# Kernel optimization log

Hardware: AMD Instinct MI355X
Metric: run time of the kernel (lower is better)

Reference implementation:

```python
import jax, jax.numpy as jnp
import numpy as np

B, N, D, H, L = 8, 128, 512, 8, 2
DK = D // H
FF = 4 * D
EPS = 1e-5  # torch LayerNorm default


def _ln(x, g, b):
    m = jnp.mean(x, axis=-1, keepdims=True)
    v = jnp.mean((x - m) ** 2, axis=-1, keepdims=True)
    return (x - m) * jax.lax.rsqrt(v + EPS) * g + b


def setup_inputs() -> dict:
    key = jax.random.key(0)
    ks = iter(jax.random.split(key, 48))
    s = 0.02

    def w(shape):
        return s * jax.random.normal(next(ks), shape, jnp.float32)

    inp = {
        "node_features": jax.random.normal(next(ks), (B, N, D), jnp.float32),
        "edge_features": jax.random.normal(next(ks), (B, N, N, D), jnp.float32),
        "adjacency": (jax.random.uniform(next(ks), (B, N, N)) < 0.3).astype(jnp.float32),
    }
    for name, shape in [("Wq", (L, D, D)), ("Wk", (L, D, D)), ("Wv", (L, D, D)),
                        ("Wo", (L, D, D)), ("Wg", (L, D, D)),
                        ("Wf1", (L, D, FF)), ("Wf2", (L, FF, D))]:
        inp[name] = w(shape)
    for name, shape in [("bq", (L, D)), ("bk", (L, D)), ("bv", (L, D)), ("bo", (L, D)),
                        ("bg", (L, D)), ("bf1", (L, FF)), ("bf2", (L, D))]:
        inp[name] = jnp.zeros(shape, jnp.float32)
    for name in ["ln1", "ln2", "ln3"]:
        inp[name + "_g"] = jnp.ones((L, D), jnp.float32)
        inp[name + "_b"] = jnp.zeros((L, D), jnp.float32)
    return inp


def _forward(node_features, edge_features, adjacency,
             Wq, bq, Wk, bk, Wv, bv, Wo, bo, ln1_g, ln1_b,
             Wg, bg, ln2_g, ln2_b, Wf1, bf1, Wf2, bf2, ln3_g, ln3_b):
    # edge bias is the mean over the feature dim, broadcast over heads: (B,1,N,N)
    edge_bias = jnp.mean(edge_features, axis=-1)[:, None]
    # adjacency-normalized GCN operator: (A + I) / row-degree (clamped to >=1)
    adj = adjacency + jnp.eye(N, dtype=adjacency.dtype)
    adj_norm = adj / jnp.clip(jnp.sum(adj, axis=-1, keepdims=True), 1.0, None)
    scale = 1.0 / np.sqrt(DK).astype(np.float32)

    x = node_features
    for l in range(L):
        # --- multi-head graph attention (dropout = identity in eval) ---
        q = (x @ Wq[l] + bq[l]).reshape(B, N, H, DK).transpose(0, 2, 1, 3)
        k = (x @ Wk[l] + bk[l]).reshape(B, N, H, DK).transpose(0, 2, 1, 3)
        v = (x @ Wv[l] + bv[l]).reshape(B, N, H, DK).transpose(0, 2, 1, 3)
        scores = jnp.einsum('bhnd,bhmd->bhnm', q, k) * scale + edge_bias
        attn = jax.nn.softmax(scores, axis=-1)
        ctx = jnp.einsum('bhnm,bhmd->bhnd', attn, v).transpose(0, 2, 1, 3).reshape(B, N, D)
        x = _ln(x + ctx @ Wo[l] + bo[l], ln1_g[l], ln1_b[l])
        # --- GCN aggregation with residual ---
        agg = jnp.einsum('bnm,bmd->bnd', adj_norm, x)
        x = _ln(x + jax.nn.relu(agg @ Wg[l] + bg[l]), ln2_g[l], ln2_b[l])
        # --- FFN with residual ---
        f = jax.nn.relu(x @ Wf1[l] + bf1[l]) @ Wf2[l] + bf2[l]
        x = _ln(x + f, ln3_g[l], ln3_b[l])
    return x


def reference(node_features, edge_features, adjacency,
              Wq, bq, Wk, bk, Wv, bv, Wo, bo, ln1_g, ln1_b,
              Wg, bg, ln2_g, ln2_b, Wf1, bf1, Wf2, bf2, ln3_g, ln3_b):
    return _forward(node_features, edge_features, adjacency,
                    Wq, bq, Wk, bk, Wv, bv, Wo, bo, ln1_g, ln1_b,
                    Wg, bg, ln2_g, ln2_b, Wf1, bf1, Wf2, bf2, ln3_g, ln3_b)
```

## Files before the change

### kernel.cpp

```cpp
#include <hip/hip_runtime.h>

#define B_  8
#define N_  128
#define D_  512
#define H_  8
#define DK_ 64
#define FF_ 2048
#define L_  2
#define EPS_ 1e-5f

#define BND  (B_*N_*D_)
#define BNN  (B_*N_*N_)
#define BNFF (B_*N_*FF_)
#define DD   (D_*D_)
#define DFF  (D_*FF_)
#define LAYER_SHORTS (10L*DD + 4L*DFF)

typedef __attribute__((ext_vector_type(8))) short short8;
typedef __attribute__((ext_vector_type(4))) float f32x4;

__device__ __forceinline__ unsigned short bf16h(float f) {
    unsigned u = __float_as_uint(f);
    return (unsigned short)((u + 0x7FFFu + ((u >> 16) & 1u)) >> 16);
}
__device__ __forceinline__ float bf16f(unsigned short h) {
    return __uint_as_float((unsigned)h << 16);
}

__global__ __launch_bounds__(256) void edge_mean_kernel(
    const float* __restrict__ ef, float* __restrict__ eb)
{
    int wid  = (blockIdx.x * blockDim.x + threadIdx.x) >> 6;
    int lane = threadIdx.x & 63;
    if (wid >= BNN) return;
    const float* p = ef + (long)wid * D_;
    float4 a = *(const float4*)&p[lane * 4];
    float4 b = *(const float4*)&p[256 + lane * 4];
    float s = a.x + a.y + a.z + a.w + b.x + b.y + b.z + b.w;
    #pragma unroll
    for (int off = 32; off; off >>= 1) s += __shfl_xor(s, off);
    if (lane == 0) eb[wid] = s * (1.0f / (float)D_);
}

__global__ __launch_bounds__(128) void adj_norm_kernel(
    const float* __restrict__ adj, float* __restrict__ an)
{
    int bi = blockIdx.x;
    int j  = threadIdx.x;
    int i  = bi & (N_ - 1);
    const float* row = adj + (long)bi * N_;
    float v = row[j] + (j == i ? 1.0f : 0.0f);
    float s = v;
    #pragma unroll
    for (int off = 32; off; off >>= 1) s += __shfl_xor(s, off);
    __shared__ float partial[2];
    if ((threadIdx.x & 63) == 0) partial[threadIdx.x >> 6] = s;
    __syncthreads();
    float tot = partial[0] + partial[1];
    tot = fmaxf(tot, 1.0f);
    an[(long)bi * N_ + j] = v / tot;
}

__global__ __launch_bounds__(256) void wconv_kernel(
    const float* __restrict__ W, unsigned short* __restrict__ Whi,
    unsigned short* __restrict__ Wlo, int K, int N)
{
    __shared__ ushort2 tile[64][65];
    int t = threadIdx.x;
    int k0 = blockIdx.y << 6, n0 = blockIdx.x << 6;
    #pragma unroll
    for (int p = 0; p < 4; ++p) {
        int k = (t >> 4) + (p << 4);
        int n = (t & 15) << 2;
        float4 v = *(const float4*)&W[(long)(k0 + k) * N + n0 + n];
        float vv[4] = {v.x, v.y, v.z, v.w};
        #pragma unroll
        for (int j = 0; j < 4; ++j) {
            unsigned short h = bf16h(vv[j]);
            unsigned short l = bf16h(vv[j] - bf16f(h));
            tile[k][n + j] = make_ushort2(h, l);
        }
    }
    __syncthreads();
    #pragma unroll
    for (int p = 0; p < 4; ++p) {
        int n = (t >> 4) + (p << 4);
        int k = (t & 15) << 2;
        ushort2 e0 = tile[k][n], e1 = tile[k + 1][n];
        ushort2 e2 = tile[k + 2][n], e3 = tile[k + 3][n];
        *(ushort4*)&Whi[(long)(n0 + n) * K + k0 + k] = make_ushort4(e0.x, e1.x, e2.x, e3.x);
        *(ushort4*)&Wlo[(long)(n0 + n) * K + k0 + k] = make_ushort4(e0.y, e1.y, e2.y, e3.y);
    }
}

__global__ __launch_bounds__(256) void gemm_mfma_kernel(
    const float* __restrict__ A,
    const unsigned short* __restrict__ WTbase, long wstride,
    const float* __restrict__ bias0, const float* __restrict__ bias1,
    const float* __restrict__ bias2,
    float* __restrict__ C, long cstride,
    int M, int N, int K, int relu)
{
    __shared__ __align__(16) unsigned short Ah[64][40];
    __shared__ __align__(16) unsigned short Al[64][40];

    int t = threadIdx.x;
    int z = blockIdx.z;
    const unsigned short* Whi = WTbase + (long)z * wstride;
    const unsigned short* Wlo = Whi + (long)N * K;
    const float* bias = (z == 0) ? bias0 : (z == 1 ? bias1 : bias2);
    float* Cb = C + (long)z * cstride;

    int m0 = blockIdx.y << 6, n0 = blockIdx.x << 6;
    int wv = t >> 6, lane = t & 63;
    int lr = lane & 15, lk = lane >> 4;

    int sr = t >> 2;
    int sk = (t & 3) << 3;
    const float* Ap = &A[(long)(m0 + sr) * K + sk];

    f32x4 acc[4] = {{0.f,0.f,0.f,0.f},{0.f,0.f,0.f,0.f},
                    {0.f,0.f,0.f,0.f},{0.f,0.f,0.f,0.f}};

    for (int k0 = 0; k0 < K; k0 += 32) {
        float4 va = *(const float4*)(Ap + k0);
        float4 vb = *(const float4*)(Ap + k0 + 4);
        float f[8] = {va.x, va.y, va.z, va.w, vb.x, vb.y, vb.z, vb.w};
        unsigned short hh[8], ll[8];
        #pragma unroll
        for (int i = 0; i < 8; ++i) {
            hh[i] = bf16h(f[i]);
            ll[i] = bf16h(f[i] - bf16f(hh[i]));
        }
        __syncthreads();
        *(ushort4*)&Ah[sr][sk]     = make_ushort4(hh[0], hh[1], hh[2], hh[3]);
        *(ushort4*)&Ah[sr][sk + 4] = make_ushort4(hh[4], hh[5], hh[6], hh[7]);
        *(ushort4*)&Al[sr][sk]     = make_ushort4(ll[0], ll[1], ll[2], ll[3]);
        *(ushort4*)&Al[sr][sk + 4] = make_ushort4(ll[4], ll[5], ll[6], ll[7]);
        __syncthreads();

        short8 ah = *(const short8*)&Ah[(wv << 4) + lr][lk << 3];
        short8 al = *(const short8*)&Al[(wv << 4) + lr][lk << 3];
        #pragma unroll
        for (int nf = 0; nf < 4; ++nf) {
            long off = (long)(n0 + (nf << 4) + lr) * K + k0 + (lk << 3);
            short8 bh = *(const short8*)(Whi + off);
            short8 bl = *(const short8*)(Wlo + off);
            acc[nf] = __builtin_amdgcn_mfma_f32_16x16x32_bf16(ah, bh, acc[nf], 0, 0, 0);
            acc[nf] = __builtin_amdgcn_mfma_f32_16x16x32_bf16(ah, bl, acc[nf], 0, 0, 0);
            acc[nf] = __builtin_amdgcn_mfma_f32_16x16x32_bf16(al, bh, acc[nf], 0, 0, 0);
        }
    }

    #pragma unroll
    for (int nf = 0; nf < 4; ++nf) {
        int col = n0 + (nf << 4) + lr;
        float bi = bias ? bias[col] : 0.f;
        #pragma unroll
        for (int r = 0; r < 4; ++r) {
            int row = m0 + (wv << 4) + (lk << 2) + r;
            float o = acc[nf][r] + bi;
            if (relu) o = fmaxf(o, 0.f);
            Cb[(long)row * N + col] = o;
        }
    }
}

__global__ __launch_bounds__(256) void gemm_kernel(
    const float* __restrict__ A, const float* __restrict__ W,
    const float* __restrict__ bias, float* __restrict__ C,
    int M, int N, int K,
    long sA, long sW, long sC, int relu)
{
    __shared__ float As[16][64];
    __shared__ float Bs[16][64];

    int tid = threadIdx.x;
    int bx = blockIdx.x, by = blockIdx.y, bz = blockIdx.z;
    const float* Ab = A + (long)bz * sA;
    const float* Wb = W + (long)bz * sW;
    float*       Cb = C + (long)bz * sC;

    int tx = tid & 15, ty = tid >> 4;
    int arow = tid >> 2, acol = (tid & 3) * 4;
    int brow = tid >> 4, bcol = (tid & 15) * 4;

    float acc[4][4] = {};

    for (int k0 = 0; k0 < K; k0 += 16) {
        float4 av = *(const float4*)&Ab[(long)(by * 64 + arow) * K + k0 + acol];
        float4 bv = *(const float4*)&Wb[(long)(k0 + brow) * N + bx * 64 + bcol];
        __syncthreads();
        As[acol + 0][arow] = av.x;
        As[acol + 1][arow] = av.y;
        As[acol + 2][arow] = av.z;
        As[acol + 3][arow] = av.w;
        *(float4*)&Bs[brow][bcol] = bv;
        __syncthreads();
        #pragma unroll
        for (int kk = 0; kk < 16; ++kk) {
            float a0 = As[kk][ty * 4 + 0];
            float a1 = As[kk][ty * 4 + 1];
            float a2 = As[kk][ty * 4 + 2];
            float a3 = As[kk][ty * 4 + 3];
            float4 b = *(float4*)&Bs[kk][tx * 4];
            acc[0][0] += a0 * b.x; acc[0][1] += a0 * b.y; acc[0][2] += a0 * b.z; acc[0][3] += a0 * b.w;
            acc[1][0] += a1 * b.x; acc[1][1] += a1 * b.y; acc[1][2] += a1 * b.z; acc[1][3] += a1 * b.w;
            acc[2][0] += a2 * b.x; acc[2][1] += a2 * b.y; acc[2][2] += a2 * b.z; acc[2][3] += a2 * b.w;
            acc[3][0] += a3 * b.x; acc[3][1] += a3 * b.y; acc[3][2] += a3 * b.z; acc[3][3] += a3 * b.w;
        }
    }

    int col = bx * 64 + tx * 4;
    float4 bo = {0.f, 0.f, 0.f, 0.f};
    if (bias) bo = *(const float4*)&bias[col];
    #pragma unroll
    for (int i = 0; i < 4; ++i) {
        int row = by * 64 + ty * 4 + i;
        float4 o;
        o.x = acc[i][0] + bo.x;
        o.y = acc[i][1] + bo.y;
        o.z = acc[i][2] + bo.z;
        o.w = acc[i][3] + bo.w;
        if (relu) {
            o.x = fmaxf(o.x, 0.f); o.y = fmaxf(o.y, 0.f);
            o.z = fmaxf(o.z, 0.f); o.w = fmaxf(o.w, 0.f);
        }
        *(float4*)&Cb[(long)row * N + col] = o;
    }
}

#define LDP 129
__global__ __launch_bounds__(256) void attn_kernel(
    const float* __restrict__ q, const float* __restrict__ k,
    const float* __restrict__ v, const float* __restrict__ eb,
    float* __restrict__ ctx)
{
    __shared__ float KT[DK_][LDP];
    __shared__ float Vs[N_][DK_];
    __shared__ float qs[2][DK_];
    __shared__ float ps[2][N_];
    __shared__ float red[2][2];
    __shared__ float cpar[2][2][DK_];

    int bh = blockIdx.x;
    int rg = blockIdx.y;
    int b  = bh >> 3, hh = bh & 7;
    int t  = threadIdx.x;

    {
        int d  = t & 63;
        int jb = t >> 6;
        const float* kb = k + ((long)b * N_) * D_ + hh * DK_;
        const float* vb = v + ((long)b * N_) * D_ + hh * DK_;
        for (int j = jb; j < N_; j += 4) {
            KT[d][j] = kb[(long)j * D_ + d];
            Vs[j][d] = vb[(long)j * D_ + d];
        }
    }
    __syncthreads();

    int sub  = t >> 7;
    int j    = t & 127;
    int lane = t & 63;
    int wh   = (t >> 6) & 1;
    int d    = t & 63;
    const float scale = 0.125f;

    for (int it = 0; it < 16; ++it) {
        int row0 = rg * 32 + it * 2;
        if (t < 128)
            qs[t >> 6][t & 63] =
                q[((long)b * N_ + row0 + (t >> 6)) * D_ + hh * DK_ + (t & 63)];
        __syncthreads();

        int row = row0 + sub;
        float s = 0.f;
        #pragma unroll
        for (int dd = 0; dd < DK_; ++dd) s += qs[sub][dd] * KT[dd][j];
        s = s * scale + eb[((long)b * N_ + row) * N_ + j];

        float m = s;
        #pragma unroll
        for (int off = 32; off; off >>= 1) m = fmaxf(m, __shfl_xor(m, off));
        if (lane == 0) red[sub][wh] = m;
        __syncthreads();
        m = fmaxf(red[sub][0], red[sub][1]);

        float p  = expf(s - m);
        float su = p;
        #pragma unroll
        for (int off = 32; off; off >>= 1) su += __shfl_xor(su, off);
        __syncthreads();
        if (lane == 0) red[sub][wh] = su;
        __syncthreads();
        su = red[sub][0] + red[sub][1];

        ps[sub][j] = p / su;
        __syncthreads();

        float acc = 0.f;
        int j0 = wh * 64;
        #pragma unroll
        for (int jj = 0; jj < 64; ++jj) acc += ps[sub][j0 + jj] * Vs[j0 + jj][d];
        cpar[sub][wh][d] = acc;
        __syncthreads();
        if (wh == 0)
            ctx[((long)b * N_ + row) * D_ + hh * DK_ + d] =
                cpar[sub][0][d] + cpar[sub][1][d];
        __syncthreads();
    }
}

__global__ __launch_bounds__(64) void ln_residual_kernel(
    float* __restrict__ x, const float* __restrict__ y,
    const float* __restrict__ g, const float* __restrict__ bb)
{
    int row  = blockIdx.x;
    int lane = threadIdx.x;
    float* xr = x + (long)row * D_;
    const float* yr = y + (long)row * D_;

    float4 a0 = *(const float4*)&xr[lane * 4];
    float4 a1 = *(const float4*)&xr[256 + lane * 4];
    float4 b0 = *(const float4*)&yr[lane * 4];
    float4 b1 = *(const float4*)&yr[256 + lane * 4];

    float v0[8] = {a0.x + b0.x, a0.y + b0.y, a0.z + b0.z, a0.w + b0.w,
                   a1.x + b1.x, a1.y + b1.y, a1.z + b1.z, a1.w + b1.w};

    float s1 = 0.f, s2 = 0.f;
    #pragma unroll
    for (int i = 0; i < 8; ++i) { s1 += v0[i]; s2 += v0[i] * v0[i]; }
    #pragma unroll
    for (int off = 32; off; off >>= 1) {
        s1 += __shfl_xor(s1, off);
        s2 += __shfl_xor(s2, off);
    }
    float mean = s1 * (1.0f / (float)D_);
    float var  = s2 * (1.0f / (float)D_) - mean * mean;
    float rstd = rsqrtf(var + EPS_);

    float4 g0 = *(const float4*)&g[lane * 4];
    float4 g1 = *(const float4*)&g[256 + lane * 4];
    float4 q0 = *(const float4*)&bb[lane * 4];
    float4 q1 = *(const float4*)&bb[256 + lane * 4];

    float4 o0, o1;
    o0.x = (v0[0] - mean) * rstd * g0.x + q0.x;
    o0.y = (v0[1] - mean) * rstd * g0.y + q0.y;
    o0.z = (v0[2] - mean) * rstd * g0.z + q0.z;
    o0.w = (v0[3] - mean) * rstd * g0.w + q0.w;
    o1.x = (v0[4] - mean) * rstd * g1.x + q1.x;
    o1.y = (v0[5] - mean) * rstd * g1.y + q1.y;
    o1.z = (v0[6] - mean) * rstd * g1.z + q1.z;
    o1.w = (v0[7] - mean) * rstd * g1.w + q1.w;

    *(float4*)&xr[lane * 4]       = o0;
    *(float4*)&xr[256 + lane * 4] = o1;
}

extern "C" void kernel_launch(void* const* d_in, const int* in_sizes, int n_in,
                              void* d_out, int out_size, void* d_ws, size_t ws_size,
                              hipStream_t stream)
{
    const float* node = (const float*)d_in[0];
    const float* edge = (const float*)d_in[1];
    const float* adj  = (const float*)d_in[2];
    const float* Wq = (const float*)d_in[3];
    const float* Wk = (const float*)d_in[4];
    const float* Wv = (const float*)d_in[5];
    const float* Wo = (const float*)d_in[6];
    const float* Wg = (const float*)d_in[7];
    const float* Wf1 = (const float*)d_in[8];
    const float* Wf2 = (const float*)d_in[9];
    const float* bq = (const float*)d_in[10];
    const float* bk = (const float*)d_in[11];
    const float* bv = (const float*)d_in[12];
    const float* bo = (const float*)d_in[13];
    const float* bg = (const float*)d_in[14];
    const float* bf1 = (const float*)d_in[15];
    const float* bf2 = (const float*)d_in[16];
    const float* ln1g = (const float*)d_in[17];
    const float* ln1b = (const float*)d_in[18];
    const float* ln2g = (const float*)d_in[19];
    const float* ln2b = (const float*)d_in[20];
    const float* ln3g = (const float*)d_in[21];
    const float* ln3b = (const float*)d_in[22];

    float* x  = (float*)d_out;
    float* ws = (float*)d_ws;
    float* eb   = ws;
    float* an   = eb + BNN;
    float* q    = an + BNN;
    float* kk   = q + BND;
    float* vv   = kk + BND;
    float* ctx  = vv + BND;
    float* hbuf = q;
    float* tbuf = ctx + BND;
    unsigned short* wcv = (unsigned short*)(tbuf + BND);

    hipMemcpyAsync(x, node, (size_t)BND * sizeof(float),
                   hipMemcpyDeviceToDevice, stream);

    edge_mean_kernel<<<BNN / 4, 256, 0, stream>>>(edge, eb);
    adj_norm_kernel<<<B_ * N_, 128, 0, stream>>>(adj, an);

    for (int l = 0; l < L_; ++l) {
        unsigned short* wl = wcv + (long)l * LAYER_SHORTS;
        unsigned short* WQT = wl;
        unsigned short* WKT = wl + 2L * DD;
        unsigned short* WVT = wl + 4L * DD;
        unsigned short* WOT = wl + 6L * DD;
        unsigned short* WGT = wl + 8L * DD;
        unsigned short* WF1T = wl + 10L * DD;
        unsigned short* WF2T = wl + 10L * DD + 2L * DFF;
        wconv_kernel<<<dim3(8, 8), 256, 0, stream>>>(Wq + (long)l * DD, WQT, WQT + DD, D_, D_);
        wconv_kernel<<<dim3(8, 8), 256, 0, stream>>>(Wk + (long)l * DD, WKT, WKT + DD, D_, D_);
        wconv_kernel<<<dim3(8, 8), 256, 0, stream>>>(Wv + (long)l * DD, WVT, WVT + DD, D_, D_);
        wconv_kernel<<<dim3(8, 8), 256, 0, stream>>>(Wo + (long)l * DD, WOT, WOT + DD, D_, D_);
        wconv_kernel<<<dim3(8, 8), 256, 0, stream>>>(Wg + (long)l * DD, WGT, WGT + DD, D_, D_);
        wconv_kernel<<<dim3(32, 8), 256, 0, stream>>>(Wf1 + (long)l * DFF, WF1T, WF1T + DFF, D_, FF_);
        wconv_kernel<<<dim3(8, 32), 256, 0, stream>>>(Wf2 + (long)l * DFF, WF2T, WF2T + DFF, FF_, D_);
    }

    const int M = B_ * N_;

    for (int l = 0; l < L_; ++l) {
        unsigned short* wl = wcv + (long)l * LAYER_SHORTS;
        unsigned short* WQT = wl;
        unsigned short* WOT = wl + 6L * DD;
        unsigned short* WGT = wl + 8L * DD;
        unsigned short* WF1T = wl + 10L * DD;
        unsigned short* WF2T = wl + 10L * DD + 2L * DFF;

        gemm_mfma_kernel<<<dim3(D_ / 64, M / 64, 3), 256, 0, stream>>>(
            x, WQT, 2L * DD, bq + l * D_, bk + l * D_, bv + l * D_,
            q, (long)BND, M, D_, D_, 0);

        attn_kernel<<<dim3(B_ * H_, 4, 1), 256, 0, stream>>>(q, kk, vv, eb, ctx);

        gemm_mfma_kernel<<<dim3(D_ / 64, M / 64, 1), 256, 0, stream>>>(
            ctx, WOT, 0, bo + l * D_, bo + l * D_, bo + l * D_,
            tbuf, 0, M, D_, D_, 0);
        ln_residual_kernel<<<M, 64, 0, stream>>>(x, tbuf, ln1g + l * D_, ln1b + l * D_);

        gemm_kernel<<<dim3(D_ / 64, N_ / 64, B_), 256, 0, stream>>>(
            an, x, nullptr, tbuf, N_, D_, N_,
            (long)N_ * N_, (long)N_ * D_, (long)N_ * D_, 0);
        gemm_mfma_kernel<<<dim3(D_ / 64, M / 64, 1), 256, 0, stream>>>(
            tbuf, WGT, 0, bg + l * D_, bg + l * D_, bg + l * D_,
            ctx, 0, M, D_, D_, 1);
        ln_residual_kernel<<<M, 64, 0, stream>>>(x, ctx, ln2g + l * D_, ln2b + l * D_);

        gemm_mfma_kernel<<<dim3(FF_ / 64, M / 64, 1), 256, 0, stream>>>(
            x, WF1T, 0, bf1 + l * FF_, bf1 + l * FF_, bf1 + l * FF_,
            hbuf, 0, M, FF_, D_, 1);
        gemm_mfma_kernel<<<dim3(D_ / 64, M / 64, 1), 256, 0, stream>>>(
            hbuf, WF2T, 0, bf2 + l * D_, bf2 + l * D_, bf2 + l * D_,
            tbuf, 0, M, D_, FF_, 0);
        ln_residual_kernel<<<M, 64, 0, stream>>>(x, tbuf, ln3g + l * D_, ln3b + l * D_);
    }
}
```

Before: 1.066 ms.

## Double-buffer MFMA GEMM A tiles, halve M tile, batch weight conversions

```diff
diff --git a/kernel.cpp b/kernel.cpp
--- a/kernel.cpp
+++ b/kernel.cpp
@@ -61,13 +61,11 @@
     an[(long)bi * N_ + j] = v / tot;
 }
 
-__global__ __launch_bounds__(256) void wconv_kernel(
+__device__ __forceinline__ void wconv_tile(
     const float* __restrict__ W, unsigned short* __restrict__ Whi,
-    unsigned short* __restrict__ Wlo, int K, int N)
+    unsigned short* __restrict__ Wlo, int K, int N, int k0, int n0, int t)
 {
     __shared__ ushort2 tile[64][65];
-    int t = threadIdx.x;
-    int k0 = blockIdx.y << 6, n0 = blockIdx.x << 6;
     #pragma unroll
     for (int p = 0; p < 4; ++p) {
         int k = (t >> 4) + (p << 4);
@@ -93,6 +91,32 @@
     }
 }
 
+__global__ __launch_bounds__(256) void wconv10_kernel(
+    const float* __restrict__ Wq, const float* __restrict__ Wk,
+    const float* __restrict__ Wv, const float* __restrict__ Wo,
+    const float* __restrict__ Wg, unsigned short* __restrict__ wcv)
+{
+    int z  = blockIdx.z;
+    int ti = z >> 1, l = z & 1;
+    const float* src = (ti == 0) ? Wq : (ti == 1) ? Wk : (ti == 2) ? Wv
+                       : (ti == 3) ? Wo : Wg;
+    src += (long)l * DD;
+    unsigned short* dh = wcv + (long)l * LAYER_SHORTS + (long)ti * 2L * DD;
+    wconv_tile(src, dh, dh + DD, D_, D_,
+               blockIdx.y << 6, blockIdx.x << 6, threadIdx.x);
+}
+
+__global__ __launch_bounds__(256) void wconvz_kernel(
+    const float* __restrict__ W, long sstride,
+    unsigned short* __restrict__ dbase, long dstride, int K, int N)
+{
+    int z = blockIdx.z;
+    const float* src = W + (long)z * sstride;
+    unsigned short* dh = dbase + (long)z * dstride;
+    wconv_tile(src, dh, dh + (long)K * N, K, N,
+               blockIdx.y << 6, blockIdx.x << 6, threadIdx.x);
+}
+
 __global__ __launch_bounds__(256) void gemm_mfma_kernel(
     const float* __restrict__ A,
     const unsigned short* __restrict__ WTbase, long wstride,
@@ -101,8 +125,8 @@
     float* __restrict__ C, long cstride,
     int M, int N, int K, int relu)
 {
-    __shared__ __align__(16) unsigned short Ah[64][40];
-    __shared__ __align__(16) unsigned short Al[64][40];
+    __shared__ __align__(16) unsigned short Ah[2][32][40];
+    __shared__ __align__(16) unsigned short Al[2][32][40];
 
     int t = threadIdx.x;
     int z = blockIdx.z;
@@ -111,54 +135,70 @@
     const float* bias = (z == 0) ? bias0 : (z == 1 ? bias1 : bias2);
     float* Cb = C + (long)z * cstride;
 
-    int m0 = blockIdx.y << 6, n0 = blockIdx.x << 6;
+    int m0 = blockIdx.y << 5, n0 = blockIdx.x << 6;
     int wv = t >> 6, lane = t & 63;
     int lr = lane & 15, lk = lane >> 4;
-
-    int sr = t >> 2;
-    int sk = (t & 3) << 3;
+    int r0 = (wv & 1) << 4;
+    int c0 = (wv >> 1) << 5;
+
+    int sr = t >> 3;
+    int sk = (t & 7) << 2;
     const float* Ap = &A[(long)(m0 + sr) * K + sk];
 
-    f32x4 acc[4] = {{0.f,0.f,0.f,0.f},{0.f,0.f,0.f,0.f},
-                    {0.f,0.f,0.f,0.f},{0.f,0.f,0.f,0.f}};
-
+    f32x4 acc[2] = {{0.f,0.f,0.f,0.f},{0.f,0.f,0.f,0.f}};
+
+    float4 va = *(const float4*)(Ap);
+    {
+        unsigned short h0 = bf16h(va.x), h1 = bf16h(va.y),
+                       h2 = bf16h(va.z), h3 = bf16h(va.w);
+        unsigned short l0 = bf16h(va.x - bf16f(h0));
+        unsigned short l1 = bf16h(va.y - bf16f(h1));
+        unsigned short l2 = bf16h(va.z - bf16f(h2));
+        unsigned short l3 = bf16h(va.w - bf16f(h3));
+        *(ushort4*)&Ah[0][sr][sk] = make_ushort4(h0, h1, h2, h3);
+        *(ushort4*)&Al[0][sr][sk] = make_ushort4(l0, l1, l2, l3);
+    }
+    __syncthreads();
+
+    int cur = 0;
     for (int k0 = 0; k0 < K; k0 += 32) {
-        float4 va = *(const float4*)(Ap + k0);
-        float4 vb = *(const float4*)(Ap + k0 + 4);
-        float f[8] = {va.x, va.y, va.z, va.w, vb.x, vb.y, vb.z, vb.w};
-        unsigned short hh[8], ll[8];
-        #pragma unroll
-        for (int i = 0; i < 8; ++i) {
-            hh[i] = bf16h(f[i]);
-            ll[i] = bf16h(f[i] - bf16f(hh[i]));
-        }
-        __syncthreads();
-        *(ushort4*)&Ah[sr][sk]     = make_ushort4(hh[0], hh[1], hh[2], hh[3]);
-        *(ushort4*)&Ah[sr][sk + 4] = make_ushort4(hh[4], hh[5], hh[6], hh[7]);
-        *(ushort4*)&Al[sr][sk]     = make_ushort4(ll[0], ll[1], ll[2], ll[3]);
-        *(ushort4*)&Al[sr][sk + 4] = make_ushort4(ll[4], ll[5], ll[6], ll[7]);
-        __syncthreads();
-
-        short8 ah = *(const short8*)&Ah[(wv << 4) + lr][lk << 3];
-        short8 al = *(const short8*)&Al[(wv << 4) + lr][lk << 3];
-        #pragma unroll
-        for (int nf = 0; nf < 4; ++nf) {
-            long off = (long)(n0 + (nf << 4) + lr) * K + k0 + (lk << 3);
+        bool more = (k0 + 32) < K;
+        if (more) va = *(const float4*)(Ap + k0 + 32);
+
+        short8 ah = *(const short8*)&Ah[cur][r0 + lr][lk << 3];
+        short8 al = *(const short8*)&Al[cur][r0 + lr][lk << 3];
+        #pragma unroll
+        for (int nf = 0; nf < 2; ++nf) {
+            long off = (long)(n0 + c0 + (nf << 4) + lr) * K + k0 + (lk << 3);
             short8 bh = *(const short8*)(Whi + off);
             short8 bl = *(const short8*)(Wlo + off);
             acc[nf] = __builtin_amdgcn_mfma_f32_16x16x32_bf16(ah, bh, acc[nf], 0, 0, 0);
             acc[nf] = __builtin_amdgcn_mfma_f32_16x16x32_bf16(ah, bl, acc[nf], 0, 0, 0);
             acc[nf] = __builtin_amdgcn_mfma_f32_16x16x32_bf16(al, bh, acc[nf], 0, 0, 0);
         }
-    }
-
-    #pragma unroll
-    for (int nf = 0; nf < 4; ++nf) {
-        int col = n0 + (nf << 4) + lr;
+
+        if (more) {
+            unsigned short h0 = bf16h(va.x), h1 = bf16h(va.y),
+                           h2 = bf16h(va.z), h3 = bf16h(va.w);
+            unsigned short l0 = bf16h(va.x - bf16f(h0));
+            unsigned short l1 = bf16h(va.y - bf16f(h1));
+            unsigned short l2 = bf16h(va.z - bf16f(h2));
+            unsigned short l3 = bf16h(va.w - bf16f(h3));
+            int nb = cur ^ 1;
+            *(ushort4*)&Ah[nb][sr][sk] = make_ushort4(h0, h1, h2, h3);
+            *(ushort4*)&Al[nb][sr][sk] = make_ushort4(l0, l1, l2, l3);
+            __syncthreads();
+            cur = nb;
+        }
+    }
+
+    #pragma unroll
+    for (int nf = 0; nf < 2; ++nf) {
+        int col = n0 + c0 + (nf << 4) + lr;
         float bi = bias ? bias[col] : 0.f;
         #pragma unroll
         for (int r = 0; r < 4; ++r) {
-            int row = m0 + (wv << 4) + (lk << 2) + r;
+            int row = m0 + r0 + (lk << 2) + r;
             float o = acc[nf][r] + bi;
             if (relu) o = fmaxf(o, 0.f);
             Cb[(long)row * N + col] = o;
@@ -406,23 +446,11 @@
     edge_mean_kernel<<<BNN / 4, 256, 0, stream>>>(edge, eb);
     adj_norm_kernel<<<B_ * N_, 128, 0, stream>>>(adj, an);
 
-    for (int l = 0; l < L_; ++l) {
-        unsigned short* wl = wcv + (long)l * LAYER_SHORTS;
-        unsigned short* WQT = wl;
-        unsigned short* WKT = wl + 2L * DD;
-        unsigned short* WVT = wl + 4L * DD;
-        unsigned short* WOT = wl + 6L * DD;
-        unsigned short* WGT = wl + 8L * DD;
-        unsigned short* WF1T = wl + 10L * DD;
-        unsigned short* WF2T = wl + 10L * DD + 2L * DFF;
-        wconv_kernel<<<dim3(8, 8), 256, 0, stream>>>(Wq + (long)l * DD, WQT, WQT + DD, D_, D_);
-        wconv_kernel<<<dim3(8, 8), 256, 0, stream>>>(Wk + (long)l * DD, WKT, WKT + DD, D_, D_);
-        wconv_kernel<<<dim3(8, 8), 256, 0, stream>>>(Wv + (long)l * DD, WVT, WVT + DD, D_, D_);
-        wconv_kernel<<<dim3(8, 8), 256, 0, stream>>>(Wo + (long)l * DD, WOT, WOT + DD, D_, D_);
-        wconv_kernel<<<dim3(8, 8), 256, 0, stream>>>(Wg + (long)l * DD, WGT, WGT + DD, D_, D_);
-        wconv_kernel<<<dim3(32, 8), 256, 0, stream>>>(Wf1 + (long)l * DFF, WF1T, WF1T + DFF, D_, FF_);
-        wconv_kernel<<<dim3(8, 32), 256, 0, stream>>>(Wf2 + (long)l * DFF, WF2T, WF2T + DFF, FF_, D_);
-    }
+    wconv10_kernel<<<dim3(8, 8, 10), 256, 0, stream>>>(Wq, Wk, Wv, Wo, Wg, wcv);
+    wconvz_kernel<<<dim3(32, 8, 2), 256, 0, stream>>>(
+        Wf1, (long)DFF, wcv + 10L * DD, (long)LAYER_SHORTS, D_, FF_);
+    wconvz_kernel<<<dim3(8, 32, 2), 256, 0, stream>>>(
+        Wf2, (long)DFF, wcv + 10L * DD + 2L * DFF, (long)LAYER_SHORTS, FF_, D_);
 
     const int M = B_ * N_;
 
@@ -434,13 +462,13 @@
         unsigned short* WF1T = wl + 10L * DD;
         unsigned short* WF2T = wl + 10L * DD + 2L * DFF;
 
-        gemm_mfma_kernel<<<dim3(D_ / 64, M / 64, 3), 256, 0, stream>>>(
+        gemm_mfma_kernel<<<dim3(D_ / 64, M / 32, 3), 256, 0, stream>>>(
             x, WQT, 2L * DD, bq + l * D_, bk + l * D_, bv + l * D_,
             q, (long)BND, M, D_, D_, 0);
 
         attn_kernel<<<dim3(B_ * H_, 4, 1), 256, 0, stream>>>(q, kk, vv, eb, ctx);
 
-        gemm_mfma_kernel<<<dim3(D_ / 64, M / 64, 1), 256, 0, stream>>>(
+        gemm_mfma_kernel<<<dim3(D_ / 64, M / 32, 1), 256, 0, stream>>>(
             ctx, WOT, 0, bo + l * D_, bo + l * D_, bo + l * D_,
             tbuf, 0, M, D_, D_, 0);
         ln_residual_kernel<<<M, 64, 0, stream>>>(x, tbuf, ln1g + l * D_, ln1b + l * D_);
@@ -448,15 +476,15 @@
         gemm_kernel<<<dim3(D_ / 64, N_ / 64, B_), 256, 0, stream>>>(
             an, x, nullptr, tbuf, N_, D_, N_,
             (long)N_ * N_, (long)N_ * D_, (long)N_ * D_, 0);
-        gemm_mfma_kernel<<<dim3(D_ / 64, M / 64, 1), 256, 0, stream>>>(
+        gemm_mfma_kernel<<<dim3(D_ / 64, M / 32, 1), 256, 0, stream>>>(
             tbuf, WGT, 0, bg + l * D_, bg + l * D_, bg + l * D_,
             ctx, 0, M, D_, D_, 1);
         ln_residual_kernel<<<M, 64, 0, stream>>>(x, ctx, ln2g + l * D_, ln2b + l * D_);
 
-        gemm_mfma_kernel<<<dim3(FF_ / 64, M / 64, 1), 256, 0, stream>>>(
+        gemm_mfma_kernel<<<dim3(FF_ / 64, M / 32, 1), 256, 0, stream>>>(
             x, WF1T, 0, bf1 + l * FF_, bf1 + l * FF_, bf1 + l * FF_,
             hbuf, 0, M, FF_, D_, 1);
-        gemm_mfma_kernel<<<dim3(D_ / 64, M / 64, 1), 256, 0, stream>>>(
+        gemm_mfma_kernel<<<dim3(D_ / 64, M / 32, 1), 256, 0, stream>>>(
             hbuf, WF2T, 0, bf2 + l * D_, bf2 + l * D_, bf2 + l * D_,
             tbuf, 0, M, D_, FF_, 0);
         ln_residual_kernel<<<M, 64, 0, stream>>>(x, tbuf, ln3g + l * D_, ln3b + l * D_);
```

After: 891.0 us. -16.4%, faster.
